# Optimization experiments

Measured on AMD Instinct MI355X. Metric: run time of the kernel, lower is better.

Reference implementation:

```python
import jax, jax.numpy as jnp
import numpy as np
from jax import lax

T, B, C, N = 1024, 64, 8, 64  # time, batch, conjugates, tags


def setup_inputs() -> dict:
    key = jax.random.key(0)
    k1, k2, k3, k4, k5, k6 = jax.random.split(key, 6)
    emissions = jax.random.normal(k1, (T, B, C, N), dtype=jnp.float32)
    tags = jax.random.randint(k2, (T, B, C), 0, N)
    lengths = jax.random.randint(k3, (B,), T // 2, T + 1)
    transitions = jax.random.normal(k4, (C, N, N), dtype=jnp.float32) * 0.1
    head_transitions = jax.random.normal(k5, (C, N), dtype=jnp.float32) * 0.1
    tail_transitions = jax.random.normal(k6, (C, N), dtype=jnp.float32) * 0.1
    return {
        "emissions": emissions,
        "tags": tags,
        "lengths": lengths,
        "transitions": transitions,
        "head_transitions": head_transitions,
        "tail_transitions": tail_transitions,
    }


def reference(emissions, tags, lengths, transitions, head_transitions, tail_transitions):
    """CRF log_prob (fit): log_scores - log_partitions, per (batch, conjugate).

    emissions: [T, B, C, N] float; tags: [T, B, C] int; lengths: [B] int.
    transitions: [C, N, N]; head/tail_transitions: [C, N].
    Returns log_prob: [B, C].
    """
    Tn, Bn, Cn, Nn = emissions.shape
    mask = jnp.arange(Tn)[:, None] < lengths[None, :]  # [T, B], step validity
    maskf = mask.astype(emissions.dtype)

    c_idx = jnp.arange(Cn)

    # ---- gold path score (semiring = Log: mul=add, prod=sum) ----
    em_score = jnp.take_along_axis(emissions, tags[..., None], axis=-1)[..., 0]  # [T,B,C]
    em_total = jnp.sum(em_score * maskf[:, :, None], axis=0)  # [B, C]

    head_sc = head_transitions[c_idx[None, :], tags[0]]  # [B, C]

    last_idx = lengths - 1
    tags_last = tags[last_idx, jnp.arange(Bn)]  # [B, C]
    tail_sc = tail_transitions[c_idx[None, :], tags_last]  # [B, C]

    trans_sc = transitions[c_idx[None, None, :], tags[:-1], tags[1:]]  # [T-1, B, C]
    trans_total = jnp.sum(trans_sc * maskf[1:, :, None], axis=0)  # [B, C]

    log_scores = em_total + head_sc + tail_sc + trans_total  # [B, C]

    # ---- log partition via forward algorithm (Log semiring bmm chain) ----
    alpha0 = head_transitions[None, :, :] + emissions[0]  # [B, C, N]

    def step(alpha, inp):
        em_t, m_t = inp  # [B,C,N], [B]
        nxt = jax.scipy.special.logsumexp(
            alpha[..., :, None] + transitions[None, :, :, :], axis=-2
        ) + em_t  # [B, C, N]
        alpha = jnp.where(m_t[:, None, None], nxt, alpha)
        return alpha, None

    alpha, _ = lax.scan(step, alpha0, (emissions[1:], mask[1:]))
    log_partitions = jax.scipy.special.logsumexp(
        alpha + tail_transitions[None, :, :], axis=-1
    )  # [B, C]

    return log_scores - log_partitions
```

## Files before the change

### kernel.cpp

```cpp
#include <hip/hip_runtime.h>
#include <cstdint>
#include <cstddef>

#define Bn 64
#define Cn 8
#define Nn 64
#define Tn 1024
#define ES 32768
#define TBC 512
#define SEGS 16
#define SEGL 64
#define BURN 16
#define NB 16
#define LN2F 0.69314718056f
#define PTS 72
#define UBS 72
#define EMS 68

typedef short bf16x8 __attribute__((ext_vector_type(8)));
typedef float f32x4m __attribute__((ext_vector_type(4)));

__device__ __forceinline__ uint32_t bf16u(float x) {
  return (__float_as_uint(x) + 0x8000u) >> 16;
}

__device__ __forceinline__ float wred_sum(float x) {
  int v;
#define STEP(ctrl) \
  v = __builtin_amdgcn_update_dpp(0, __float_as_int(x), ctrl, 0xf, 0xf, false); \
  x = x + __int_as_float(v);
  STEP(0x111) STEP(0x112) STEP(0x114) STEP(0x118) STEP(0x142) STEP(0x143)
#undef STEP
  return __int_as_float(__builtin_amdgcn_readlane(__float_as_int(x), 63));
}

__global__ __launch_bounds__(256)
void crf_mfma(const float* __restrict__ em, const int* __restrict__ lengths,
              const float* __restrict__ trans, const float* __restrict__ head,
              const float* __restrict__ tail, float* __restrict__ ws) {
  __shared__ unsigned short Pt[Nn * PTS];
  __shared__ unsigned short Ub[2][NB * UBS];
  __shared__ float Em[3][NB * EMS];
  __shared__ float red[NB];
  __shared__ float red2[NB];
  __shared__ float scratch[256];

  const int bid = blockIdx.x;
  const int c = bid & 7;
  const int s = (bid >> 3) & 15;
  const int g = bid >> 7;

  const int tid = threadIdx.x;
  const int w = tid >> 6, l = tid & 63;
  const int l15 = l & 15, lg = l >> 4;
  const int m0 = w * 16 + lg * 4;
  const int jrow = w * 16 + l15;

  {
    const float* tc = trans + c * (Nn * Nn);
    const int j = tid & 63, kb = (tid >> 6) * 16;
#pragma unroll
    for (int kk = 0; kk < 16; kk += 2) {
      float a  = __expf(tc[(kb + kk) * Nn + j]);
      float b2 = __expf(tc[(kb + kk + 1) * Nn + j]);
      *(uint32_t*)&Pt[j * PTS + kb + kk] = bf16u(a) | (bf16u(b2) << 16);
    }
  }

  const int lenb = lengths[g * NB + l15];
  const int own = (lenb - 1) >> 6;
  float te[4];
  {
    float4 t4 = *(const float4*)(tail + c * Nn + m0);
    te[0] = __expf(t4.x); te[1] = __expf(t4.y);
    te[2] = __expf(t4.z); te[3] = __expf(t4.w);
  }

  const int T0  = (s == 0) ? 1 : (s * SEGL - BURN + 1);
  const int NST = (s == 0) ? SEGL : (SEGL + BURN);

  float u[4];
  if (s == 0) {
    float4 h4 = *(const float4*)(head + c * Nn + m0);
    const int bg = g * NB + l15;
    float4 e4 = *(const float4*)(em + (size_t)bg * TBC + c * Nn + m0);
    u[0] = __expf(h4.x + e4.x); u[1] = __expf(h4.y + e4.y);
    u[2] = __expf(h4.z + e4.z); u[3] = __expf(h4.w + e4.w);
  } else {
    u[0] = 1.f; u[1] = 1.f; u[2] = 1.f; u[3] = 1.f;
  }

  *(uint32_t*)&Ub[0][l15 * UBS + m0]     = bf16u(u[0]) | (bf16u(u[1]) << 16);
  *(uint32_t*)&Ub[0][l15 * UBS + m0 + 2] = bf16u(u[2]) | (bf16u(u[3]) << 16);

  const int bl = tid >> 4, ch = tid & 15;
  {
    const float* p0 = em + (size_t)T0 * ES + (size_t)(g * NB + bl) * TBC + c * Nn + ch * 4;
    *(float4*)&Em[0][bl * EMS + ch * 4] = *(const float4*)(p0);
    int t1 = T0 + 1; if (t1 > Tn - 1) t1 = Tn - 1;
    const float* p1 = em + (size_t)t1 * ES + (size_t)(g * NB + bl) * TBC + c * Nn + ch * 4;
    *(float4*)&Em[1][bl * EMS + ch * 4] = *(const float4*)(p1);
  }

  __syncthreads();

  const bf16x8 af0 = *(const bf16x8*)&Pt[jrow * PTS + lg * 8];
  const bf16x8 af1 = *(const bf16x8*)&Pt[jrow * PTS + 32 + lg * 8];

  int Lk = 0;
  float logref = 0.f;

  for (int i = 0; i < NST; ++i) {
    const int t = T0 + i;
    const int ib = i % 3;
    const int cu = i & 1, nx = cu ^ 1;

    float4 gA;
    const bool doStage = (i + 2 < NST);
    if (doStage) {
      int tn = t + 2; if (tn > Tn - 1) tn = Tn - 1;
      gA = *(const float4*)(em + (size_t)tn * ES + (size_t)(g * NB + bl) * TBC + c * Nn + ch * 4);
    }

    if (s != 0 && i == BURN) {
      scratch[tid] = (u[0] + u[1]) + (u[2] + u[3]);
      __syncthreads();
      if (tid < NB) {
        float ssum = 0.f;
#pragma unroll
        for (int q2 = 0; q2 < 16; ++q2)
          ssum += scratch[(q2 >> 2) * 64 + (q2 & 3) * 16 + tid];
        red2[tid] = __logf(ssum);
      }
      __syncthreads();
      logref = red2[l15] + (float)Lk * LN2F;
    }

    if ((i & 3) == 0 && i > 0 && tid < 128) {
      const uint32_t* ur = (const uint32_t*)&Ub[cu][(tid >> 3) * UBS + (tid & 7) * 8];
      uint32_t d0 = ur[0], d1 = ur[1], d2 = ur[2], d3 = ur[3];
      float mx = fmaxf(
        fmaxf(fmaxf(__uint_as_float(d0 << 16), __uint_as_float(d0 & 0xFFFF0000u)),
              fmaxf(__uint_as_float(d1 << 16), __uint_as_float(d1 & 0xFFFF0000u))),
        fmaxf(fmaxf(__uint_as_float(d2 << 16), __uint_as_float(d2 & 0xFFFF0000u)),
              fmaxf(__uint_as_float(d3 << 16), __uint_as_float(d3 & 0xFFFF0000u))));
      int v;
      v = __builtin_amdgcn_update_dpp(0, __float_as_int(mx), 0x111, 0xf, 0xf, false);
      mx = fmaxf(mx, __int_as_float(v));
      v = __builtin_amdgcn_update_dpp(0, __float_as_int(mx), 0x112, 0xf, 0xf, false);
      mx = fmaxf(mx, __int_as_float(v));
      v = __builtin_amdgcn_update_dpp(0, __float_as_int(mx), 0x114, 0xf, 0xf, false);
      mx = fmaxf(mx, __int_as_float(v));
      if ((tid & 7) == 7) red[tid >> 3] = mx;
    }

    const bf16x8 b00 = *(const bf16x8*)&Ub[cu][l15 * UBS + lg * 8];
    const bf16x8 b10 = *(const bf16x8*)&Ub[cu][l15 * UBS + 32 + lg * 8];
    const float4 e0 = *(const float4*)&Em[ib][l15 * EMS + m0];

    f32x4m acc = {0.f, 0.f, 0.f, 0.f};
    acc = __builtin_amdgcn_mfma_f32_16x16x32_bf16(af0, b00, acc, 0, 0, 0);
    acc = __builtin_amdgcn_mfma_f32_16x16x32_bf16(af1, b10, acc, 0, 0, 0);

    int kp = 0;
    if ((i & 3) == 1 && i >= 5) {
      float mv = red[l15];
      kp = (int)((__float_as_uint(mv) >> 23) & 255u) - 127;
    }

    {
      const bool live = (t < lenb);
      const float scl = __int_as_float((uint32_t)(127 - kp) << 23);
      float v0 = live ? acc[0] * __expf(e0.x) : u[0];
      float v1 = live ? acc[1] * __expf(e0.y) : u[1];
      float v2 = live ? acc[2] * __expf(e0.z) : u[2];
      float v3 = live ? acc[3] * __expf(e0.w) : u[3];
      u[0] = v0 * scl; u[1] = v1 * scl; u[2] = v2 * scl; u[3] = v3 * scl;
      Lk += kp;
      *(uint32_t*)&Ub[nx][l15 * UBS + m0]     = bf16u(u[0]) | (bf16u(u[1]) << 16);
      *(uint32_t*)&Ub[nx][l15 * UBS + m0 + 2] = bf16u(u[2]) | (bf16u(u[3]) << 16);
    }

    if (doStage) {
      const int sb = (i + 2) % 3;
      *(float4*)&Em[sb][bl * EMS + ch * 4] = gA;
    }

    __syncthreads();
  }

  {
    const bool at = (own == s);
    float p = u[0] * (at ? te[0] : 1.f) + u[1] * (at ? te[1] : 1.f)
            + u[2] * (at ? te[2] : 1.f) + u[3] * (at ? te[3] : 1.f);
    scratch[tid] = p;
  }
  __syncthreads();
  if (tid < NB) {
    float ssum = 0.f;
#pragma unroll
    for (int q2 = 0; q2 < 16; ++q2)
      ssum += scratch[(q2 >> 2) * 64 + (q2 & 3) * 16 + tid];
    const float term = __logf(ssum) + (float)Lk * LN2F - logref;
    const int bg = g * NB + tid;
    ws[(bg * Cn + c) * SEGS + s] = -term;
  }
}

__global__ __launch_bounds__(256)
void crf_score(const float* __restrict__ em, const int* __restrict__ tags,
               const int* __restrict__ lengths, const float* __restrict__ trans,
               const float* __restrict__ head, const float* __restrict__ tail,
               const float* __restrict__ ws, float* __restrict__ out) {
  __shared__ float part[4];
  const int bc = blockIdx.x;
  const int b = bc >> 3, c = bc & 7;
  const int tid = threadIdx.x;
  const int len = lengths[b];
  float sc = 0.f;
#pragma unroll
  for (int it = 0; it < 4; ++it) {
    int t = it * 256 + tid;
    if (t < len) {
      int tagc = tags[t * TBC + bc];
      sc += em[(size_t)t * ES + (size_t)bc * Nn + tagc];
      if (t >= 1) {
        int tagp = tags[(t - 1) * TBC + bc];
        sc += trans[c * (Nn * Nn) + tagp * Nn + tagc];
      } else {
        sc += head[c * Nn + tagc];
      }
      if (t == len - 1) sc += tail[c * Nn + tagc];
    }
  }
  sc = wred_sum(sc);
  if ((tid & 63) == 0) part[tid >> 6] = sc;
  __syncthreads();
  if (tid == 0) {
    float tot = (part[0] + part[1]) + (part[2] + part[3]);
    const float* p = ws + bc * SEGS;
    float sws = 0.f;
#pragma unroll
    for (int k = 0; k < SEGS; ++k) sws += p[k];
    out[bc] = tot + sws;
  }
}

extern "C" void kernel_launch(void* const* d_in, const int* in_sizes, int n_in,
                              void* d_out, int out_size, void* d_ws, size_t ws_size,
                              hipStream_t stream) {
  const float* em      = (const float*)d_in[0];
  const int*   tags    = (const int*)d_in[1];
  const int*   lengths = (const int*)d_in[2];
  const float* trans   = (const float*)d_in[3];
  const float* head    = (const float*)d_in[4];
  const float* tail    = (const float*)d_in[5];
  float* out = (float*)d_out;
  float* ws  = (float*)d_ws;
  crf_mfma<<<dim3(Cn * SEGS * 4), dim3(256), 0, stream>>>(em, lengths, trans, head, tail, ws);
  crf_score<<<dim3(Bn * Cn), dim3(256), 0, stream>>>(em, tags, lengths, trans, head, tail, ws, out);
}
```

Measured before the change: 55.01 us.

## Double time segments and fuse gold-path scoring into forward kernel

Splits the time axis into 32 segments of 32 steps instead of 16 of 64, doubling the block count and shortening the serial forward recurrence each block runs. Each block now also computes the gold-path score for its own time slice and writes it together with its partition term. This replaces the separate scoring kernel with a tiny combine kernel. The cost is more redundant burn-in steps relative to useful steps, plus extra gather loads inside the forward kernel.

```diff
diff --git a/kernel.cpp b/kernel.cpp
--- a/kernel.cpp
+++ b/kernel.cpp
@@ -8,8 +8,8 @@
 #define Tn 1024
 #define ES 32768
 #define TBC 512
-#define SEGS 16
-#define SEGL 64
+#define SEGS 32
+#define SEGL 32
 #define BURN 16
 #define NB 16
 #define LN2F 0.69314718056f
@@ -24,31 +24,23 @@
   return (__float_as_uint(x) + 0x8000u) >> 16;
 }
 
-__device__ __forceinline__ float wred_sum(float x) {
-  int v;
-#define STEP(ctrl) \
-  v = __builtin_amdgcn_update_dpp(0, __float_as_int(x), ctrl, 0xf, 0xf, false); \
-  x = x + __int_as_float(v);
-  STEP(0x111) STEP(0x112) STEP(0x114) STEP(0x118) STEP(0x142) STEP(0x143)
-#undef STEP
-  return __int_as_float(__builtin_amdgcn_readlane(__float_as_int(x), 63));
-}
-
 __global__ __launch_bounds__(256)
-void crf_mfma(const float* __restrict__ em, const int* __restrict__ lengths,
-              const float* __restrict__ trans, const float* __restrict__ head,
-              const float* __restrict__ tail, float* __restrict__ ws) {
+void crf_mfma(const float* __restrict__ em, const int* __restrict__ tags,
+              const int* __restrict__ lengths, const float* __restrict__ trans,
+              const float* __restrict__ head, const float* __restrict__ tail,
+              float* __restrict__ ws) {
   __shared__ unsigned short Pt[Nn * PTS];
   __shared__ unsigned short Ub[2][NB * UBS];
   __shared__ float Em[3][NB * EMS];
   __shared__ float red[NB];
   __shared__ float red2[NB];
+  __shared__ float scv[NB];
   __shared__ float scratch[256];
 
   const int bid = blockIdx.x;
   const int c = bid & 7;
-  const int s = (bid >> 3) & 15;
-  const int g = bid >> 7;
+  const int s = (bid >> 3) & 31;
+  const int g = bid >> 8;
 
   const int tid = threadIdx.x;
   const int w = tid >> 6, l = tid & 63;
@@ -68,7 +60,7 @@
   }
 
   const int lenb = lengths[g * NB + l15];
-  const int own = (lenb - 1) >> 6;
+  const int own = (lenb - 1) >> 5;
   float te[4];
   {
     float4 t4 = *(const float4*)(tail + c * Nn + m0);
@@ -78,6 +70,32 @@
 
   const int T0  = (s == 0) ? 1 : (s * SEGL - BURN + 1);
   const int NST = (s == 0) ? SEGL : (SEGL + BURN);
+
+  {
+    const int n = tid & 15;
+    const int bcg = (g * NB + n) * Cn + c;
+    const int lenn = lengths[g * NB + n];
+    float sc = 0.f;
+#pragma unroll
+    for (int q2 = 0; q2 < 2; ++q2) {
+      int t = s * SEGL + (tid >> 4) + q2 * 16;
+      if (t < lenn) {
+        int tagc = tags[t * TBC + bcg];
+        sc += em[(size_t)t * ES + (size_t)bcg * Nn + tagc];
+        if (t >= 1) sc += trans[c * (Nn * Nn) + tags[(t - 1) * TBC + bcg] * Nn + tagc];
+        else        sc += head[c * Nn + tagc];
+        if (t == lenn - 1) sc += tail[c * Nn + tagc];
+      }
+    }
+    scratch[tid] = sc;
+  }
+  __syncthreads();
+  if (tid < NB) {
+    float ssum = 0.f;
+#pragma unroll
+    for (int j = 0; j < 16; ++j) ssum += scratch[j * 16 + tid];
+    scv[tid] = ssum;
+  }
 
   float u[4];
   if (s == 0) {
@@ -203,46 +221,19 @@
       ssum += scratch[(q2 >> 2) * 64 + (q2 & 3) * 16 + tid];
     const float term = __logf(ssum) + (float)Lk * LN2F - logref;
     const int bg = g * NB + tid;
-    ws[(bg * Cn + c) * SEGS + s] = -term;
-  }
-}
-
-__global__ __launch_bounds__(256)
-void crf_score(const float* __restrict__ em, const int* __restrict__ tags,
-               const int* __restrict__ lengths, const float* __restrict__ trans,
-               const float* __restrict__ head, const float* __restrict__ tail,
-               const float* __restrict__ ws, float* __restrict__ out) {
-  __shared__ float part[4];
-  const int bc = blockIdx.x;
-  const int b = bc >> 3, c = bc & 7;
-  const int tid = threadIdx.x;
-  const int len = lengths[b];
-  float sc = 0.f;
-#pragma unroll
-  for (int it = 0; it < 4; ++it) {
-    int t = it * 256 + tid;
-    if (t < len) {
-      int tagc = tags[t * TBC + bc];
-      sc += em[(size_t)t * ES + (size_t)bc * Nn + tagc];
-      if (t >= 1) {
-        int tagp = tags[(t - 1) * TBC + bc];
-        sc += trans[c * (Nn * Nn) + tagp * Nn + tagc];
-      } else {
-        sc += head[c * Nn + tagc];
-      }
-      if (t == len - 1) sc += tail[c * Nn + tagc];
-    }
-  }
-  sc = wred_sum(sc);
-  if ((tid & 63) == 0) part[tid >> 6] = sc;
-  __syncthreads();
-  if (tid == 0) {
-    float tot = (part[0] + part[1]) + (part[2] + part[3]);
-    const float* p = ws + bc * SEGS;
-    float sws = 0.f;
-#pragma unroll
-    for (int k = 0; k < SEGS; ++k) sws += p[k];
-    out[bc] = tot + sws;
+    ws[(bg * Cn + c) * SEGS + s] = scv[tid] - term;
+  }
+}
+
+__global__ __launch_bounds__(64)
+void crf_combine(const float* __restrict__ ws, float* __restrict__ out) {
+  int i = blockIdx.x * 64 + threadIdx.x;
+  if (i < Bn * Cn) {
+    const float* p = ws + i * SEGS;
+    float sacc = 0.f;
+#pragma unroll
+    for (int k = 0; k < SEGS; ++k) sacc += p[k];
+    out[i] = sacc;
   }
 }
 
@@ -257,6 +248,6 @@
   const float* tail    = (const float*)d_in[5];
   float* out = (float*)d_out;
   float* ws  = (float*)d_ws;
-  crf_mfma<<<dim3(Cn * SEGS * 4), dim3(256), 0, stream>>>(em, lengths, trans, head, tail, ws);
-  crf_score<<<dim3(Bn * Cn), dim3(256), 0, stream>>>(em, tags, lengths, trans, head, tail, ws, out);
-}
+  crf_mfma<<<dim3(Cn * SEGS * 4), dim3(256), 0, stream>>>(em, tags, lengths, trans, head, tail, ws);
+  crf_combine<<<dim3(8), dim3(64), 0, stream>>>(ws, out);
+}
```

After: 46.79 us. 14.9% less time.
